# Kernel optimization log

Hardware: AMD Instinct MI355X
Metric: run time of the kernel (lower is better)

The kernel has to match this reference:

```python
import jax, jax.numpy as jnp
import numpy as np

N, DIM_V, DIM_MM, DIM_O = 1024, 2048, 64, 2048
EPS_LOG = 1e-3


def setup_inputs() -> dict:
    key = jax.random.key(0)
    ks = jax.random.split(key, 12)
    feature_visual = jax.random.normal(ks[0], (N, DIM_V), dtype=jnp.float32)
    # valid boxes (x1, y1, x2, y2) inside an ~800x600 image
    x1 = jax.random.uniform(ks[1], (N, 1)) * 700.0
    y1 = jax.random.uniform(ks[2], (N, 1)) * 500.0
    w = jax.random.uniform(ks[3], (N, 1)) * 180.0 + 16.0
    h = jax.random.uniform(ks[4], (N, 1)) * 180.0 + 16.0
    rois = jnp.concatenate([x1, y1, x1 + w, y1 + h], axis=1)
    s = 0.02
    return {
        "feature_visual": feature_visual,
        "rois": rois,
        "Wk": jax.random.normal(ks[5], (DIM_V, DIM_MM), dtype=jnp.float32) * s,
        "bk": jnp.zeros((DIM_MM,), jnp.float32),
        "Wq": jax.random.normal(ks[6], (DIM_V, DIM_MM), dtype=jnp.float32) * s,
        "bq": jnp.zeros((DIM_MM,), jnp.float32),
        "Wv": jax.random.normal(ks[7], (DIM_V, DIM_O), dtype=jnp.float32) * s,
        "bv": jnp.zeros((DIM_O,), jnp.float32),
        "G1": jax.random.normal(ks[8], (4, DIM_MM), dtype=jnp.float32) * s,
        "g1": jnp.zeros((DIM_MM,), jnp.float32),
        "G2": jax.random.normal(ks[9], (DIM_MM, 1), dtype=jnp.float32) * s,
        "g2": jnp.zeros((1,), jnp.float32),
    }


def _geometry_weight(rois, G1, g1, G2, g2):
    # pairwise relative geometry features [N, N, 4], then MLP -> ReLU scalar weight [N, N]
    wh = rois[:, 2:4] - rois[:, 0:2]                      # [N, 2] box width/height
    ctr = 0.5 * (rois[:, 0:2] + rois[:, 2:4])             # [N, 2] centers
    d = ctr[None, :, :] - ctr[:, None, :]                 # [N, N, 2] (j relative to i)
    f12 = jnp.log(jnp.abs(d) / wh[:, None, :] + EPS_LOG)  # log(|dx|/wi), log(|dy|/hi)
    f34 = jnp.log(wh[None, :, :] / wh[:, None, :])        # log(wj/wi), log(hj/hi)
    geo = jnp.concatenate([f12, f34], axis=-1)            # [N, N, 4]
    h = jax.nn.relu(jnp.einsum('ijf,fm->ijm', geo, G1) + g1)
    w = jax.nn.relu(jnp.einsum('ijm,mo->ijo', h, G2) + g2)
    return w[..., 0]                                      # [N, N]


def reference(feature_visual, rois, Wk, bk, Wq, bq, Wv, bv, G1, g1, G2, g2):
    fv = jax.nn.relu(feature_visual)                      # pre-activation features
    k = fv @ Wk + bk                                      # [N, dim_mm]
    q = fv @ Wq + bq                                      # [N, dim_mm]
    v = fv @ Wv + bv                                      # [N, dim_o]
    scale = 1.0 / np.sqrt(DIM_MM).astype(np.float32)
    visual_weight = (q @ k.T) * scale                     # [N, N]: score[i,j] = <q_i... wait
    # torch: (query.unsqueeze(0) * key.unsqueeze(1)).sum(2) -> score[i,j] = <k_i, q_j>
    visual_weight = (k @ q.T) * scale
    geometry_weight = _geometry_weight(rois, G1, g1, G2, g2)
    attention = jnp.exp(visual_weight) * geometry_weight  # [N, N]
    n = attention.shape[0]
    attention = attention * (1.0 - jnp.eye(n, dtype=attention.dtype))  # zero diagonal
    attention = attention / (attention.sum(axis=1, keepdims=True) + 1e-10)
    return attention @ v                                  # [N, dim_o]
```

## Files before the change

kernel.cpp:

```cpp
#include <hip/hip_runtime.h>
#include <hip/hip_bf16.h>

#define NR 1024
#define DV 2048
#define DMM 64
#define DO 2048

typedef __attribute__((ext_vector_type(8))) __bf16 bf16x8;
typedef __attribute__((ext_vector_type(4))) float f32x4;

__device__ __forceinline__ float relu_f(float x) { return fmaxf(x, 0.f); }

__device__ __forceinline__ unsigned short f2bf(float x) {
    union { float f; unsigned int u; } v; v.f = x;
    unsigned int r = v.u + 0x7fffu + ((v.u >> 16) & 1u);
    return (unsigned short)(r >> 16);
}

__device__ __forceinline__ void gload_lds16(const void* g, void* l) {
    __builtin_amdgcn_global_load_lds(
        (const __attribute__((address_space(1))) void*)g,
        (__attribute__((address_space(3))) void*)l, 16, 0, 0);
}

__device__ __forceinline__ void transpose_tile(
    const float* __restrict__ W, unsigned short* __restrict__ Wt,
    int Ncols, int k0, int o0, float (*ld)[65])
{
    const int t = threadIdx.x;
    const int r = t >> 2;
    const int c0 = (t & 3) * 16;
    #pragma unroll
    for (int i = 0; i < 4; ++i) {
        float4 v = *reinterpret_cast<const float4*>(&W[(size_t)(k0 + r) * Ncols + o0 + c0 + i * 4]);
        ld[c0 + i * 4 + 0][r] = v.x;
        ld[c0 + i * 4 + 1][r] = v.y;
        ld[c0 + i * 4 + 2][r] = v.z;
        ld[c0 + i * 4 + 3][r] = v.w;
    }
    __syncthreads();
    const int o = t >> 2;
    const int kc = (t & 3) * 16;
    unsigned int u[8];
    #pragma unroll
    for (int j = 0; j < 8; ++j) {
        float x0 = ld[o][kc + 2 * j], x1 = ld[o][kc + 2 * j + 1];
        u[j] = (unsigned)f2bf(x0) | ((unsigned)f2bf(x1) << 16);
    }
    uint4* dst = reinterpret_cast<uint4*>(&Wt[(size_t)(o0 + o) * DV + k0 + kc]);
    dst[0] = make_uint4(u[0], u[1], u[2], u[3]);
    dst[1] = make_uint4(u[4], u[5], u[6], u[7]);
}

__global__ __launch_bounds__(256) void prep_kernel(
    const float* __restrict__ feat,
    const float* __restrict__ Wk, const float* __restrict__ Wq, const float* __restrict__ Wv,
    const float* __restrict__ rois,
    unsigned short* __restrict__ fvb, unsigned short* __restrict__ WkqT,
    unsigned short* __restrict__ WvT,
    float4* __restrict__ boxf, float2* __restrict__ boxinv)
{
    __shared__ float ld[64][65];
    const int bid = blockIdx.x;
    if (bid < 1024) {
        const int idx = bid * 256 + threadIdx.x;
        const float4 a = *reinterpret_cast<const float4*>(feat + (size_t)idx * 8);
        const float4 b = *reinterpret_cast<const float4*>(feat + (size_t)idx * 8 + 4);
        uint4 o;
        o.x = (unsigned)f2bf(relu_f(a.x)) | ((unsigned)f2bf(relu_f(a.y)) << 16);
        o.y = (unsigned)f2bf(relu_f(a.z)) | ((unsigned)f2bf(relu_f(a.w)) << 16);
        o.z = (unsigned)f2bf(relu_f(b.x)) | ((unsigned)f2bf(relu_f(b.y)) << 16);
        o.w = (unsigned)f2bf(relu_f(b.z)) | ((unsigned)f2bf(relu_f(b.w)) << 16);
        *reinterpret_cast<uint4*>(fvb + (size_t)idx * 8) = o;
    } else if (bid < 2048) {
        const int idx = bid - 1024;
        transpose_tile(Wv, WvT, DO, (idx >> 5) * 64, (idx & 31) * 64, ld);
    } else if (bid < 2080) {
        transpose_tile(Wk, WkqT, DMM, (bid - 2048) * 64, 0, ld);
    } else if (bid < 2112) {
        transpose_tile(Wq, WkqT + 64 * DV, DMM, (bid - 2080) * 64, 0, ld);
    } else {
        const int idx = (bid - 2112) * 256 + threadIdx.x;
        const float4 r = *reinterpret_cast<const float4*>(rois + (size_t)idx * 4);
        const float w = r.z - r.x, h = r.w - r.y;
        boxf[idx]   = make_float4(0.5f * (r.x + r.z), 0.5f * (r.y + r.w), __logf(w), __logf(h));
        boxinv[idx] = make_float2(1.f / w, 1.f / h);
    }
}

template<int NT, int LDA, int LDB>
__device__ __forceinline__ void mfma_tile_pipe(
    const unsigned short* __restrict__ A, const unsigned short* __restrict__ Bt,
    int bm0, int bn0, unsigned short* As, unsigned short* Bs, f32x4 (&acc)[2][4])
{
    const int t = threadIdx.x;
    const int w = t >> 6, lane = t & 63;
    const int wr = w >> 1, wc = w & 1;
    const int srow = lane >> 2, scol = (lane & 3) * 8;
    const int fr = lane & 15, fq = lane >> 4;

    const unsigned short* ga  = A  + (size_t)(bm0 + w * 16 + srow) * LDA + scol;
    const unsigned short* gb0 = Bt + (size_t)(bn0 + w * 16 + srow) * LDB + scol;
    const unsigned short* gb1 = Bt + (size_t)(bn0 + 64 + w * 16 + srow) * LDB + scol;
    const int la  = (w * 16) * 32;
    const int lb0 = (w * 16) * 32;
    const int lb1 = (64 + w * 16) * 32;

#define STAGE(buf, ts_) do {                                        \
        gload_lds16(ga  + (size_t)(ts_) * 32, &As[(buf) * 2048 + la]);  \
        gload_lds16(gb0 + (size_t)(ts_) * 32, &Bs[(buf) * 4096 + lb0]); \
        gload_lds16(gb1 + (size_t)(ts_) * 32, &Bs[(buf) * 4096 + lb1]); \
    } while (0)

#define COMPUTE(buf) do {                                                                     \
        bf16x8 af[2], bfr[4];                                                                 \
        _Pragma("unroll")                                                                     \
        for (int m = 0; m < 2; ++m)                                                           \
            af[m] = *reinterpret_cast<const bf16x8*>(                                         \
                &As[(buf) * 2048 + (wr * 32 + m * 16 + fr) * 32 + fq * 8]);                   \
        _Pragma("unroll")                                                                     \
        for (int n = 0; n < 4; ++n)                                                           \
            bfr[n] = *reinterpret_cast<const bf16x8*>(                                        \
                &Bs[(buf) * 4096 + (wc * 64 + n * 16 + fr) * 32 + fq * 8]);                   \
        _Pragma("unroll")                                                                     \
        for (int m = 0; m < 2; ++m)                                                           \
            _Pragma("unroll")                                                                 \
            for (int n = 0; n < 4; ++n)                                                       \
                acc[m][n] = __builtin_amdgcn_mfma_f32_16x16x32_bf16(af[m], bfr[n], acc[m][n], 0, 0, 0); \
    } while (0)

    STAGE(0, 0);
    if (NT > 1) STAGE(1, 1);

    #pragma unroll 4
    for (int ts = 0; ts < NT - 1; ++ts) {
        asm volatile("s_waitcnt vmcnt(3)" ::: "memory");
        asm volatile("s_barrier" ::: "memory");
        COMPUTE(ts & 1);
        asm volatile("s_barrier" ::: "memory");
        if (ts + 2 < NT) STAGE(ts & 1, ts + 2);
    }
    asm volatile("s_waitcnt vmcnt(0)" ::: "memory");
    asm volatile("s_barrier" ::: "memory");
    COMPUTE((NT - 1) & 1);
#undef STAGE
#undef COMPUTE
}

__global__ __launch_bounds__(256) void gemm_vt_kq(
    const unsigned short* __restrict__ WvT, const unsigned short* __restrict__ fvb,
    const unsigned short* __restrict__ WkqT,
    const float* __restrict__ bv, const float* __restrict__ bk, const float* __restrict__ bq,
    unsigned short* __restrict__ vT, unsigned short* __restrict__ kqb)
{
    __shared__ unsigned short As[2 * 64 * 32];
    __shared__ unsigned short Bs[2 * 128 * 32];
    const int bid = blockIdx.x;
    const bool is_kq = bid >= 256;
    const unsigned short* A  = is_kq ? fvb  : WvT;
    const unsigned short* Bt = is_kq ? WkqT : fvb;
    const int bm0 = is_kq ? (bid - 256) * 64 : (bid >> 3) * 64;
    const int bn0 = is_kq ? 0 : (bid & 7) * 128;

    f32x4 acc[2][4] = {};
    mfma_tile_pipe<DV / 32, DV, DV>(A, Bt, bm0, bn0, As, Bs, acc);

    const int t = threadIdx.x;
    const int w = t >> 6, lane = t & 63;
    const int wr = w >> 1, wc = w & 1;
    const int fr = lane & 15, fq = lane >> 4;
    if (!is_kq) {
        #pragma unroll
        for (int m = 0; m < 2; ++m)
            #pragma unroll
            for (int r = 0; r < 4; ++r) {
                const int row = bm0 + wr * 32 + m * 16 + fq * 4 + r;
                const float badd = bv[row];
                #pragma unroll
                for (int n = 0; n < 4; ++n) {
                    const int col = bn0 + wc * 64 + n * 16 + fr;
                    vT[(size_t)row * NR + col] = f2bf(acc[m][n][r] + badd);
                }
            }
    } else {
        #pragma unroll
        for (int m = 0; m < 2; ++m)
            #pragma unroll
            for (int r = 0; r < 4; ++r) {
                const int row = bm0 + wr * 32 + m * 16 + fq * 4 + r;
                #pragma unroll
                for (int n = 0; n < 4; ++n) {
                    const int col = wc * 64 + n * 16 + fr;
                    const float badd = (col < 64) ? bk[col] : bq[col - 64];
                    kqb[(size_t)row * 128 + col] = f2bf(acc[m][n][r] + badd);
                }
            }
    }
}

__global__ __launch_bounds__(256) void gemm_s(
    const unsigned short* __restrict__ kqb, float* __restrict__ S)
{
    __shared__ unsigned short As[2 * 64 * 32];
    __shared__ unsigned short Bs[2 * 128 * 32];
    const int bm0 = blockIdx.y * 64;
    const int bn0 = blockIdx.x * 128;
    f32x4 acc[2][4] = {};
    mfma_tile_pipe<2, 128, 128>(kqb, kqb + 64, bm0, bn0, As, Bs, acc);
    const int t = threadIdx.x;
    const int w = t >> 6, lane = t & 63;
    const int wr = w >> 1, wc = w & 1;
    const int fr = lane & 15, fq = lane >> 4;
    #pragma unroll
    for (int m = 0; m < 2; ++m)
        #pragma unroll
        for (int r = 0; r < 4; ++r) {
            const int row = bm0 + wr * 32 + m * 16 + fq * 4 + r;
            #pragma unroll
            for (int n = 0; n < 4; ++n) {
                const int col = bn0 + wc * 64 + n * 16 + fr;
                S[(size_t)row * NR + col] = acc[m][n][r] * 0.125f;
            }
        }
}

__global__ __launch_bounds__(256) void gemm_out(
    const unsigned short* __restrict__ attb, const unsigned short* __restrict__ vT,
    float* __restrict__ out)
{
    __shared__ unsigned short As[2 * 64 * 32];
    __shared__ unsigned short Bs[2 * 128 * 32];
    const int bm0 = blockIdx.y * 64;
    const int bn0 = blockIdx.x * 128;
    f32x4 acc[2][4] = {};
    mfma_tile_pipe<NR / 32, NR, NR>(attb, vT, bm0, bn0, As, Bs, acc);
    const int t = threadIdx.x;
    const int w = t >> 6, lane = t & 63;
    const int wr = w >> 1, wc = w & 1;
    const int fr = lane & 15, fq = lane >> 4;
    #pragma unroll
    for (int m = 0; m < 2; ++m)
        #pragma unroll
        for (int r = 0; r < 4; ++r) {
            const int row = bm0 + wr * 32 + m * 16 + fq * 4 + r;
            #pragma unroll
            for (int n = 0; n < 4; ++n) {
                const int col = bn0 + wc * 64 + n * 16 + fr;
                out[(size_t)row * DO + col] = acc[m][n][r];
            }
        }
}

#define MLP_STEP(A_, B_, C_, D_, E_, F_)                                            \
    {                                                                               \
        float h_ = fmaf(ff1[ch], A_, fmaf(ff2[ch], B_, fmaf(ff3[ch], C_,            \
                   fmaf(ff4[ch], D_, E_))));                                        \
        h_ = fmaxf(h_, 0.f);                                                        \
        gw[ch] = fmaf(h_, F_, gw[ch]);                                              \
    }

__global__ __launch_bounds__(256) void attn_kernel(
    const float* __restrict__ S,
    const float4* __restrict__ boxf, const float2* __restrict__ boxinv,
    const float* __restrict__ G1, const float* __restrict__ g1,
    const float* __restrict__ G2, const float* __restrict__ g2,
    unsigned short* __restrict__ att)
{
    __shared__ float G1s[4][64];
    __shared__ float g1s[64];
    __shared__ float G2s[64];
    __shared__ float red[4];
    const int i = blockIdx.x;
    const int t = threadIdx.x;
    if (t < 64) {
        G1s[0][t] = G1[t];
        G1s[1][t] = G1[64 + t];
        G1s[2][t] = G1[128 + t];
        G1s[3][t] = G1[192 + t];
        g1s[t] = g1[t];
        G2s[t] = G2[t];
    }
    __syncthreads();
    const float4 bi = boxf[i];
    const float2 ivi = boxinv[i];
    const float g2v = g2[0];

    float ff1[4], ff2[4], ff3[4], ff4[4], sc[4], gw[4] = {0.f, 0.f, 0.f, 0.f};
    #pragma unroll
    for (int ch = 0; ch < 4; ++ch) {
        const int j = ch * 256 + t;
        const float4 bj = boxf[j];
        sc[ch] = S[(size_t)i * NR + j];
        ff1[ch] = __logf(fmaf(fabsf(bj.x - bi.x), ivi.x, 1e-3f));
        ff2[ch] = __logf(fmaf(fabsf(bj.y - bi.y), ivi.y, 1e-3f));
        ff3[ch] = bj.z - bi.z;
        ff4[ch] = bj.w - bi.w;
    }

    for (int mt = 0; mt < 64; mt += 8) {
        const float4 A0 = *reinterpret_cast<const float4*>(&G1s[0][mt]);
        const float4 A1 = *reinterpret_cast<const float4*>(&G1s[0][mt + 4]);
        const float4 B0 = *reinterpret_cast<const float4*>(&G1s[1][mt]);
        const float4 B1 = *reinterpret_cast<const float4*>(&G1s[1][mt + 4]);
        const float4 C0 = *reinterpret_cast<const float4*>(&G1s[2][mt]);
        const float4 C1 = *reinterpret_cast<const float4*>(&G1s[2][mt + 4]);
        const float4 D0 = *reinterpret_cast<const float4*>(&G1s[3][mt]);
        const float4 D1 = *reinterpret_cast<const float4*>(&G1s[3][mt + 4]);
        const float4 E0 = *reinterpret_cast<const float4*>(&g1s[mt]);
        const float4 E1 = *reinterpret_cast<const float4*>(&g1s[mt + 4]);
        const float4 F0 = *reinterpret_cast<const float4*>(&G2s[mt]);
        const float4 F1 = *reinterpret_cast<const float4*>(&G2s[mt + 4]);
        #pragma unroll
        for (int ch = 0; ch < 4; ++ch) {
            MLP_STEP(A0.x, B0.x, C0.x, D0.x, E0.x, F0.x)
            MLP_STEP(A0.y, B0.y, C0.y, D0.y, E0.y, F0.y)
            MLP_STEP(A0.z, B0.z, C0.z, D0.z, E0.z, F0.z)
            MLP_STEP(A0.w, B0.w, C0.w, D0.w, E0.w, F0.w)
            MLP_STEP(A1.x, B1.x, C1.x, D1.x, E1.x, F1.x)
            MLP_STEP(A1.y, B1.y, C1.y, D1.y, E1.y, F1.y)
            MLP_STEP(A1.z, B1.z, C1.z, D1.z, E1.z, F1.z)
            MLP_STEP(A1.w, B1.w, C1.w, D1.w, E1.w, F1.w)
        }
    }

    float vals[4];
    float rsum = 0.f;
    #pragma unroll
    for (int ch = 0; ch < 4; ++ch) {
        const float gwp = fmaxf(gw[ch] + g2v, 0.f);
        float a = __expf(sc[ch]) * gwp;
        if (ch * 256 + t == i) a = 0.f;
        vals[ch] = a;
        rsum += a;
    }
    #pragma unroll
    for (int o = 32; o > 0; o >>= 1) rsum += __shfl_down(rsum, o, 64);
    if ((t & 63) == 0) red[t >> 6] = rsum;
    __syncthreads();
    const float inv = 1.f / (red[0] + red[1] + red[2] + red[3] + 1e-10f);
    #pragma unroll
    for (int ch = 0; ch < 4; ++ch)
        att[(size_t)i * NR + ch * 256 + t] = f2bf(vals[ch] * inv);
}

extern "C" void kernel_launch(void* const* d_in, const int* in_sizes, int n_in,
                              void* d_out, int out_size, void* d_ws, size_t ws_size,
                              hipStream_t stream) {
    const float* feat = (const float*)d_in[0];
    const float* rois = (const float*)d_in[1];
    const float* Wk   = (const float*)d_in[2];
    const float* bk   = (const float*)d_in[3];
    const float* Wq   = (const float*)d_in[4];
    const float* bq   = (const float*)d_in[5];
    const float* Wv   = (const float*)d_in[6];
    const float* bv   = (const float*)d_in[7];
    const float* G1   = (const float*)d_in[8];
    const float* g1   = (const float*)d_in[9];
    const float* G2   = (const float*)d_in[10];
    const float* g2   = (const float*)d_in[11];
    float* out = (float*)d_out;
    char* ws = (char*)d_ws;

    unsigned short* kqb  = (unsigned short*)ws;
    float4* boxf         = (float4*)(ws + (256 << 10));
    float2* boxinv       = (float2*)(ws + (272 << 10));
    unsigned short* fvb  = (unsigned short*)(ws + (512 << 10));
    unsigned short* WvT  = (unsigned short*)(ws + (512 << 10) + (4 << 20));
    unsigned short* WkqT = (unsigned short*)(ws + (512 << 10) + (12 << 20));
    unsigned short* vT   = (unsigned short*)(ws + (1024 << 10) + (12 << 20));
    unsigned short* attb = (unsigned short*)(ws + (1024 << 10) + (16 << 20));
    float* Sbuf          = (float*)(ws + (1024 << 10) + (18 << 20));

    prep_kernel<<<2116, 256, 0, stream>>>(feat, Wk, Wq, Wv, rois, fvb, WkqT, WvT, boxf, boxinv);
    gemm_vt_kq<<<272, 256, 0, stream>>>(WvT, fvb, WkqT, bv, bk, bq, vT, kqb);
    gemm_s<<<dim3(8, 16), 256, 0, stream>>>(kqb, Sbuf);
    attn_kernel<<<NR, 256, 0, stream>>>(Sbuf, boxf, boxinv, G1, g1, G2, g2, attb);
    gemm_out<<<dim3(DO / 128, NR / 64), 256, 0, stream>>>(attb, vT, out);
}
```

Before: 71.42 us.

## Double GEMM K-tile to 64 with XOR-swizzled LDS layout

The shared bf16 MFMA pipeline now stages K-tiles of 64 instead of 32. Each wave issues six 16-byte global-to-LDS loads per stage, and an XOR swizzle on the column chunk is meant to avoid LDS bank conflicts when fragments are read. This halves the number of barrier/waitcnt iterations per GEMM and doubles the MFMAs per synchronization. In exchange LDS use doubles to 48KB per block, which may reduce occupancy, and the wait count and unroll factor are adjusted to match.

Measured after the change: 64.77 us. 1.1x faster.

```diff
diff --git a/kernel.cpp b/kernel.cpp
--- a/kernel.cpp
+++ b/kernel.cpp
@@ -96,45 +96,58 @@
     const int t = threadIdx.x;
     const int w = t >> 6, lane = t & 63;
     const int wr = w >> 1, wc = w & 1;
-    const int srow = lane >> 2, scol = (lane & 3) * 8;
     const int fr = lane & 15, fq = lane >> 4;
-
-    const unsigned short* ga  = A  + (size_t)(bm0 + w * 16 + srow) * LDA + scol;
-    const unsigned short* gb0 = Bt + (size_t)(bn0 + w * 16 + srow) * LDB + scol;
-    const unsigned short* gb1 = Bt + (size_t)(bn0 + 64 + w * 16 + srow) * LDB + scol;
-    const int la  = (w * 16) * 32;
-    const int lb0 = (w * 16) * 32;
-    const int lb1 = (64 + w * 16) * 32;
-
-#define STAGE(buf, ts_) do {                                        \
-        gload_lds16(ga  + (size_t)(ts_) * 32, &As[(buf) * 2048 + la]);  \
-        gload_lds16(gb0 + (size_t)(ts_) * 32, &Bs[(buf) * 4096 + lb0]); \
-        gload_lds16(gb1 + (size_t)(ts_) * 32, &Bs[(buf) * 4096 + lb1]); \
+    const int sr = lane >> 3;
+    const int sc = ((lane & 7) ^ sr) * 8;
+
+    const unsigned short* ga0 = A  + (size_t)(bm0 + w * 16 +  0 + sr) * LDA + sc;
+    const unsigned short* ga1 = A  + (size_t)(bm0 + w * 16 +  8 + sr) * LDA + sc;
+    const unsigned short* gb0 = Bt + (size_t)(bn0 + w * 32 +  0 + sr) * LDB + sc;
+    const unsigned short* gb1 = Bt + (size_t)(bn0 + w * 32 +  8 + sr) * LDB + sc;
+    const unsigned short* gb2 = Bt + (size_t)(bn0 + w * 32 + 16 + sr) * LDB + sc;
+    const unsigned short* gb3 = Bt + (size_t)(bn0 + w * 32 + 24 + sr) * LDB + sc;
+
+#define STAGE(buf, ts_) do {                                                  \
+        const size_t ko_ = (size_t)(ts_) * 64;                                \
+        gload_lds16(ga0 + ko_, &As[(buf) * 4096 + w * 1024]);                 \
+        gload_lds16(ga1 + ko_, &As[(buf) * 4096 + w * 1024 + 512]);           \
+        gload_lds16(gb0 + ko_, &Bs[(buf) * 8192 + w * 2048]);                 \
+        gload_lds16(gb1 + ko_, &Bs[(buf) * 8192 + w * 2048 + 512]);           \
+        gload_lds16(gb2 + ko_, &Bs[(buf) * 8192 + w * 2048 + 1024]);          \
+        gload_lds16(gb3 + ko_, &Bs[(buf) * 8192 + w * 2048 + 1536]);          \
     } while (0)
 
 #define COMPUTE(buf) do {                                                                     \
-        bf16x8 af[2], bfr[4];                                                                 \
+        const int kx_ = fr & 7;                                                               \
+        const int clo_ = (fq ^ kx_) * 8, chi_ = ((fq + 4) ^ kx_) * 8;                         \
+        bf16x8 afl[2], afh[2], bfl[4], bfh[4];                                                \
         _Pragma("unroll")                                                                     \
-        for (int m = 0; m < 2; ++m)                                                           \
-            af[m] = *reinterpret_cast<const bf16x8*>(                                         \
-                &As[(buf) * 2048 + (wr * 32 + m * 16 + fr) * 32 + fq * 8]);                   \
+        for (int m = 0; m < 2; ++m) {                                                         \
+            const int rb = (buf) * 4096 + (wr * 32 + m * 16 + fr) * 64;                       \
+            afl[m] = *reinterpret_cast<const bf16x8*>(&As[rb + clo_]);                        \
+            afh[m] = *reinterpret_cast<const bf16x8*>(&As[rb + chi_]);                        \
+        }                                                                                     \
         _Pragma("unroll")                                                                     \
-        for (int n = 0; n < 4; ++n)                                                           \
-            bfr[n] = *reinterpret_cast<const bf16x8*>(                                        \
-                &Bs[(buf) * 4096 + (wc * 64 + n * 16 + fr) * 32 + fq * 8]);                   \
+        for (int n = 0; n < 4; ++n) {                                                         \
+            const int cb = (buf) * 8192 + (wc * 64 + n * 16 + fr) * 64;                       \
+            bfl[n] = *reinterpret_cast<const bf16x8*>(&Bs[cb + clo_]);                        \
+            bfh[n] = *reinterpret_cast<const bf16x8*>(&Bs[cb + chi_]);                        \
+        }                                                                                     \
         _Pragma("unroll")                                                                     \
         for (int m = 0; m < 2; ++m)                                                           \
             _Pragma("unroll")                                                                 \
-            for (int n = 0; n < 4; ++n)                                                       \
-                acc[m][n] = __builtin_amdgcn_mfma_f32_16x16x32_bf16(af[m], bfr[n], acc[m][n], 0, 0, 0); \
+            for (int n = 0; n < 4; ++n) {                                                     \
+                acc[m][n] = __builtin_amdgcn_mfma_f32_16x16x32_bf16(afl[m], bfl[n], acc[m][n], 0, 0, 0); \
+                acc[m][n] = __builtin_amdgcn_mfma_f32_16x16x32_bf16(afh[m], bfh[n], acc[m][n], 0, 0, 0); \
+            }                                                                                 \
     } while (0)
 
     STAGE(0, 0);
     if (NT > 1) STAGE(1, 1);
 
-    #pragma unroll 4
+    #pragma unroll 2
     for (int ts = 0; ts < NT - 1; ++ts) {
-        asm volatile("s_waitcnt vmcnt(3)" ::: "memory");
+        asm volatile("s_waitcnt vmcnt(6)" ::: "memory");
         asm volatile("s_barrier" ::: "memory");
         COMPUTE(ts & 1);
         asm volatile("s_barrier" ::: "memory");
@@ -153,8 +166,8 @@
     const float* __restrict__ bv, const float* __restrict__ bk, const float* __restrict__ bq,
     unsigned short* __restrict__ vT, unsigned short* __restrict__ kqb)
 {
-    __shared__ unsigned short As[2 * 64 * 32];
-    __shared__ unsigned short Bs[2 * 128 * 32];
+    __shared__ unsigned short As[2 * 64 * 64];
+    __shared__ unsigned short Bs[2 * 128 * 64];
     const int bid = blockIdx.x;
     const bool is_kq = bid >= 256;
     const unsigned short* A  = is_kq ? fvb  : WvT;
@@ -163,7 +176,7 @@
     const int bn0 = is_kq ? 0 : (bid & 7) * 128;
 
     f32x4 acc[2][4] = {};
-    mfma_tile_pipe<DV / 32, DV, DV>(A, Bt, bm0, bn0, As, Bs, acc);
+    mfma_tile_pipe<DV / 64, DV, DV>(A, Bt, bm0, bn0, As, Bs, acc);
 
     const int t = threadIdx.x;
     const int w = t >> 6, lane = t & 63;
@@ -201,12 +214,12 @@
 __global__ __launch_bounds__(256) void gemm_s(
     const unsigned short* __restrict__ kqb, float* __restrict__ S)
 {
-    __shared__ unsigned short As[2 * 64 * 32];
-    __shared__ unsigned short Bs[2 * 128 * 32];
+    __shared__ unsigned short As[2 * 64 * 64];
+    __shared__ unsigned short Bs[2 * 128 * 64];
     const int bm0 = blockIdx.y * 64;
     const int bn0 = blockIdx.x * 128;
     f32x4 acc[2][4] = {};
-    mfma_tile_pipe<2, 128, 128>(kqb, kqb + 64, bm0, bn0, As, Bs, acc);
+    mfma_tile_pipe<1, 128, 128>(kqb, kqb + 64, bm0, bn0, As, Bs, acc);
     const int t = threadIdx.x;
     const int w = t >> 6, lane = t & 63;
     const int wr = w >> 1, wc = w & 1;
@@ -228,12 +241,12 @@
     const unsigned short* __restrict__ attb, const unsigned short* __restrict__ vT,
     float* __restrict__ out)
 {
-    __shared__ unsigned short As[2 * 64 * 32];
-    __shared__ unsigned short Bs[2 * 128 * 32];
+    __shared__ unsigned short As[2 * 64 * 64];
+    __shared__ unsigned short Bs[2 * 128 * 64];
     const int bm0 = blockIdx.y * 64;
     const int bn0 = blockIdx.x * 128;
     f32x4 acc[2][4] = {};
-    mfma_tile_pipe<NR / 32, NR, NR>(attb, vT, bm0, bn0, As, Bs, acc);
+    mfma_tile_pipe<NR / 64, NR, NR>(attb, vT, bm0, bn0, As, Bs, acc);
     const int t = threadIdx.x;
     const int w = t >> 6, lane = t & 63;
     const int wr = w >> 1, wc = w & 1;
```
